# Performance work log

Hardware: AMD Instinct MI355X
Metric: run time of the kernel (lower is better)

The kernel has to match this reference:

```python
import jax, jax.numpy as jnp
from jax import lax
import numpy as np

DN = ('NCHW', 'OIHW', 'NCHW')
EPS = 1e-5


def conv(x, w, b, stride, pad):
    y = lax.conv_general_dilated(x, w, (stride, stride), [(pad, pad), (pad, pad)],
                                 dimension_numbers=DN)
    return y + b[None, :, None, None]


def conv_transpose(x, w, b):
    # torch ConvTranspose2d(k=4, s=2, p=1) == conv with lhs_dilation=2, pad=k-1-p=2
    y = lax.conv_general_dilated(x, w, (1, 1), [(2, 2), (2, 2)],
                                 lhs_dilation=(2, 2), dimension_numbers=DN)
    return y + b[None, :, None, None]


def group_norm(x, gamma, beta, groups):
    b, c, h, w = x.shape
    xg = x.reshape(b, groups, -1)
    mean = xg.mean(axis=2, keepdims=True)
    var = xg.var(axis=2, keepdims=True)
    xg = (xg - mean) * lax.rsqrt(var + EPS)
    x = xg.reshape(b, c, h, w)
    return x * gamma[None, :, None, None] + beta[None, :, None, None]


def silu(x):
    return x * jax.nn.sigmoid(x)


def setup_inputs() -> dict:
    key = jax.random.key(0)
    ks = iter(jax.random.split(key, 40))
    s = 0.05
    d = {}
    d['x'] = jax.random.normal(next(ks), (16, 3, 256, 256), dtype=jnp.float32)
    # encoder: 3->128->256->512 (k=4,s=2,p=1) each with GroupNorm(32)+SiLU, then 512->32 1x1
    chans = [(3, 128), (128, 256), (256, 512)]
    for i, (ci, co) in enumerate(chans):
        d[f'enc{i}_w'] = jax.random.normal(next(ks), (co, ci, 4, 4), dtype=jnp.float32) * s
        d[f'enc{i}_b'] = jnp.zeros((co,), jnp.float32)
        d[f'enc{i}_g'] = jnp.ones((co,), jnp.float32)
        d[f'enc{i}_bt'] = jnp.zeros((co,), jnp.float32)
    d['enc3_w'] = jax.random.normal(next(ks), (32, 512, 1, 1), dtype=jnp.float32) * s
    d['enc3_b'] = jnp.zeros((32,), jnp.float32)
    d['codebook'] = jax.random.normal(next(ks), (1024, 32), dtype=jnp.float32)
    # decoder: 32->512 1x1, then ConvT 512->256, 256->128 (GN+SiLU), ConvT 128->3 + tanh
    d['dec0_w'] = jax.random.normal(next(ks), (512, 32, 1, 1), dtype=jnp.float32) * s
    d['dec0_b'] = jnp.zeros((512,), jnp.float32)
    tchans = [(512, 256), (256, 128)]
    for i, (ci, co) in enumerate(tchans, start=1):
        d[f'dec{i}_w'] = jax.random.normal(next(ks), (co, ci, 4, 4), dtype=jnp.float32) * s
        d[f'dec{i}_b'] = jnp.zeros((co,), jnp.float32)
        d[f'dec{i}_g'] = jnp.ones((co,), jnp.float32)
        d[f'dec{i}_bt'] = jnp.zeros((co,), jnp.float32)
    d['dec3_w'] = jax.random.normal(next(ks), (3, 128, 4, 4), dtype=jnp.float32) * s
    d['dec3_b'] = jnp.zeros((3,), jnp.float32)
    return d


def reference(x, enc0_w, enc0_b, enc0_g, enc0_bt,
              enc1_w, enc1_b, enc1_g, enc1_bt,
              enc2_w, enc2_b, enc2_g, enc2_bt,
              enc3_w, enc3_b, codebook,
              dec0_w, dec0_b,
              dec1_w, dec1_b, dec1_g, dec1_bt,
              dec2_w, dec2_b, dec2_g, dec2_bt,
              dec3_w, dec3_b):
    # encoder
    h = silu(group_norm(conv(x, enc0_w, enc0_b, 2, 1), enc0_g, enc0_bt, 32))
    h = silu(group_norm(conv(h, enc1_w, enc1_b, 2, 1), enc1_g, enc1_bt, 32))
    h = silu(group_norm(conv(h, enc2_w, enc2_b, 2, 1), enc2_g, enc2_bt, 32))
    z = conv(h, enc3_w, enc3_b, 1, 0)          # [B, 32, 32, 32]
    b, c, hh, ww = z.shape
    zf = z.reshape(-1, c)                       # row-major flatten, as in original
    # squared-distance matrix [B*H*W, n_embeddings]
    d = (jnp.sum(zf * zf, axis=1, keepdims=True)
         + jnp.sum(codebook * codebook, axis=1)
         - 2.0 * zf @ codebook.T)
    idx = jnp.argmin(d, axis=1)
    q = codebook[idx].reshape(b, c, hh, ww)
    # decoder
    h = conv(q, dec0_w, dec0_b, 1, 0)
    h = silu(group_norm(conv_transpose(h, dec1_w, dec1_b), dec1_g, dec1_bt, 32))
    h = silu(group_norm(conv_transpose(h, dec2_w, dec2_b), dec2_g, dec2_bt, 32))
    recon = jnp.tanh(conv_transpose(h, dec3_w, dec3_b))
    return recon, q, idx
```

## Files before the change

### kernel.cpp

```cpp
#include <hip/hip_runtime.h>
#include <hip/hip_bf16.h>
#include <math.h>


#define EPS 1e-5f
typedef unsigned short ushort_t;
typedef unsigned int uint32;
typedef __attribute__((ext_vector_type(8))) short bf16x8;
typedef __attribute__((ext_vector_type(4))) float f32x4;
typedef __attribute__((ext_vector_type(4))) unsigned int u32x4;

__device__ __forceinline__ ushort_t f2bf(float x) {
    __hip_bfloat16 h = __float2bfloat16(x);
    return __builtin_bit_cast(ushort_t, h);
}
__device__ __forceinline__ float bf2f(ushort_t u) {
    __hip_bfloat16 h = __builtin_bit_cast(__hip_bfloat16, u);
    return __bfloat162float(h);
}
template <int NS>
__device__ __forceinline__ void splitNS(float x, ushort_t* p) {
    float r = x;
    #pragma unroll
    for (int s = 0; s < NS; ++s) {
        ushort_t u = f2bf(r);
        p[s] = u;
        if (s + 1 < NS) r -= bf2f(u);
    }
}

template <int Cout, int Cin>
__global__ __launch_bounds__(256) void wsplit_enc(
    const float* __restrict__ w, ushort_t* __restrict__ o)
{
    constexpr int KCH = Cin / 32, CB = Cout / 16;
    int idx = blockIdx.x * 256 + threadIdx.x;
    if (idx >= Cout * Cin * 16) return;
    int tap = idx & 15;
    int ci  = (idx >> 4) % Cin;
    int co  = (idx >> 4) / Cin;
    ushort_t sp[3];
    splitNS<3>(w[idx], sp);
    const int kc = ci >> 5, q = (ci >> 3) & 3, e = ci & 7;
    const int cb = co >> 4, l15 = co & 15;
    const int lane = q * 16 + l15;
    #pragma unroll
    for (int s = 0; s < 3; ++s)
        o[((((size_t)(s * 16 + tap) * KCH + kc) * CB + cb) * 64 + lane) * 8 + e] = sp[s];
}

template <int KCH, int CB>
__device__ __forceinline__ void ldaf2(bf16x8 (&dst)[2][3],
    const ushort_t* __restrict__ wsp_t, int kc, int tap)
{
    #pragma unroll
    for (int cf = 0; cf < 2; ++cf)
        #pragma unroll
        for (int s = 0; s < 3; ++s)
            dst[cf][s] = *(const bf16x8*)(wsp_t +
                ((size_t)((s * 16 + tap) * KCH + kc) * CB + cf) * 512);
}

template <int Cin, int Cout, int Hin, int Win>
__global__ __launch_bounds__(512, 4) void mfenc(
    const float* __restrict__ x, const ushort_t* __restrict__ wsp,
    const float* __restrict__ bias, float* __restrict__ y)
{
    constexpr int Hout = Hin / 2, Wout = Win / 2;
    constexpr int MB = 32;
    constexpr int MT = Wout / MB;
    constexpr int NCOL = 66;
    constexpr int KC = 32;
    constexpr int KCH = Cin / 32;
    constexpr int CB = Cout / 16;
    constexpr int BUFW = 3 * 4 * 4 * 68 * 8;
    __shared__ ushort_t Xs[BUFW];

    const int n  = blockIdx.z;
    const int oh = blockIdx.x / MT;
    const int mt = blockIdx.x % MT;
    const int M0 = mt * MB;
    const int co_base = blockIdx.y * 256;
    const int tid = threadIdx.x;
    const int wv = tid >> 6, lane = tid & 63;
    const int q = lane >> 4, l15 = lane & 15;
    const int co_w0 = co_base + wv * 32;
    const int cb0 = (co_base >> 4) + wv * 2;
    const ushort_t* __restrict__ wsp_t = wsp + ((size_t)cb0 * 64 + lane) * 8;

    int ro[4]; bool rv[4];
    #pragma unroll
    for (int k = 0; k < 4; ++k) {
        int r = 2 * oh - 1 + k;
        rv[k] = (r >= 0) && (r < Hin);
        ro[k] = rv[k] ? r : 0;
    }

    f32x4 acc[2][2];
    #pragma unroll
    for (int a = 0; a < 2; ++a)
        #pragma unroll
        for (int b = 0; b < 2; ++b) acc[a][b] = (f32x4){0.f, 0.f, 0.f, 0.f};

    const int p16  = tid >> 5;
    const int cg5  = tid & 31;
    const int sciq = p16 >> 2;
    const int cieP = p16 & 3;

    float a0[4][3], a1[4][3];

    auto stage_load = [&](int ci0) {
        const float* b0 = x + (size_t)(n * Cin + ci0 + 2 * p16) * Hin * Win;
        const float* b1 = b0 + (size_t)Hin * Win;
        #pragma unroll
        for (int r = 0; r < 4; ++r) {
            const float* rp0 = b0 + (size_t)ro[r] * Win;
            const float* rp1 = b1 + (size_t)ro[r] * Win;
            #pragma unroll
            for (int t = 0; t < 3; ++t) {
                const int c = cg5 + 32 * t;
                const int gc = 2 * M0 - 1 + c;
                const bool ok = rv[r] && (c < NCOL) && (gc >= 0) && (gc < Win);
                a0[r][t] = ok ? rp0[gc] : 0.f;
                a1[r][t] = ok ? rp1[gc] : 0.f;
            }
        }
    };
    auto stage_write = [&]() {
        uint32* __restrict__ dst32 = (uint32*)Xs;
        #pragma unroll
        for (int r = 0; r < 4; ++r)
            #pragma unroll
            for (int t = 0; t < 3; ++t) {
                const int c = cg5 + 32 * t;
                if (c < NCOL) {
                    ushort_t s0[3], s1[3];
                    splitNS<3>(a0[r][t], s0);
                    splitNS<3>(a1[r][t], s1);
                    const int cpos = (c >> 1) + (c & 1) * 34;
                    #pragma unroll
                    for (int s = 0; s < 3; ++s)
                        dst32[((((s * 4 + r) * 4 + sciq) * 68) + cpos) * 4 + cieP] =
                            (uint32)s0[s] | ((uint32)s1[s] << 16);
                }
            }
    };

    bf16x8 afA[2][3], afB[2][3];
    ldaf2<KCH, CB>(afA, wsp_t, 0, 0);

    stage_load(0);
    stage_write();
    __syncthreads();

    for (int kc = 0; kc < KCH; ++kc) {
        if (kc + 1 < KCH) stage_load((kc + 1) * KC);
        __builtin_amdgcn_sched_barrier(0);

        __builtin_amdgcn_s_setprio(1);
        #pragma unroll
        for (int tap = 0; tap < 16; ++tap) {
            bf16x8 (&cw)[2][3] = (tap & 1) ? afB : afA;
            bf16x8 (&nw)[2][3] = (tap & 1) ? afA : afB;
            if (tap < 15) {
                ldaf2<KCH, CB>(nw, wsp_t, kc, tap + 1);
            } else if (kc + 1 < KCH) {
                ldaf2<KCH, CB>(nw, wsp_t, kc + 1, 0);
            }

            const int kh = tap >> 2, kw = tap & 3;
            bf16x8 bx[2][3];
            const int cpbase = (kw >> 1) + (kw & 1) * 34;
            #pragma unroll
            for (int mf = 0; mf < 2; ++mf) {
                const int cpos = (mf * 16 + l15) + cpbase;
                #pragma unroll
                for (int s = 0; s < 3; ++s)
                    bx[mf][s] = *(const bf16x8*)(&Xs[((((s * 4 + kh) * 4 + q) * 68) + cpos) * 8]);
            }
            #pragma unroll
            for (int sa = 0; sa < 3; ++sa)
                #pragma unroll
                for (int sb = 0; sb < 3; ++sb) {
                    if (sa + sb >= 3) continue;
                    #pragma unroll
                    for (int cf = 0; cf < 2; ++cf)
                        #pragma unroll
                        for (int mf = 0; mf < 2; ++mf)
                            acc[cf][mf] = __builtin_amdgcn_mfma_f32_16x16x32_bf16(
                                cw[cf][sa], bx[mf][sb], acc[cf][mf], 0, 0, 0);
                }
        }
        __builtin_amdgcn_s_setprio(0);

        if (kc + 1 < KCH) {
            __syncthreads();
            stage_write();
            __syncthreads();
        }
    }

    #pragma unroll
    for (int cf = 0; cf < 2; ++cf)
        #pragma unroll
        for (int mf = 0; mf < 2; ++mf) {
            const int ow = M0 + mf * 16 + l15;
            #pragma unroll
            for (int rg = 0; rg < 4; ++rg) {
                const int co = co_w0 + cf * 16 + q * 4 + rg;
                y[(((size_t)n * Cout + co) * Hout + oh) * Wout + ow] =
                    acc[cf][mf][rg] + bias[co];
            }
        }
}

template <int Cout, int Cin>
__global__ __launch_bounds__(256) void wsplit_convt(
    const float* __restrict__ w, ushort_t* __restrict__ o)
{
    constexpr int KST = Cin / 8;
    constexpr int CB = Cout / 16;
    int idx = blockIdx.x * 256 + threadIdx.x;
    if (idx >= 4 * KST * CB * 512) return;
    const int e = idx & 7;
    const int lane = (idx >> 3) & 63;
    int rest = idx >> 9;
    const int cb = rest % CB; rest /= CB;
    const int kst = rest % KST;
    const int p = rest / KST;
    const int q = lane >> 4, l15 = lane & 15;
    const int co = cb * 16 + l15;
    const int kf = kst * 32 + q * 8 + e;
    const int ci = kf >> 2, a = (kf >> 1) & 1, b = kf & 1;
    const int di = p >> 1, dj = p & 1;
    const float v = w[(((size_t)co * Cin + ci) * 4 + (2 * a + di)) * 4 + (2 * b + dj)];
    o[idx] = f2bf(v);
}

template <int Cin, int Cout, int Hin, int Win, int CO_WAVES, int M_WAVES, int KC>
__global__ __launch_bounds__(256) void mfconvt(
    const float* __restrict__ x, const ushort_t* __restrict__ wsp,
    const float* __restrict__ bias, float* __restrict__ y)
{
    constexpr int NDp = Win / 2 + 2;
    constexpr int CO_B = CO_WAVES * 32;
    constexpr int KST = Cin / 8;
    constexpr int CB = Cout / 16;
    constexpr int KCH = Cin / KC;
    constexpr int SEGW = Win / 4;
    constexpr int SEGS = KC * 2 * SEGW;
    constexpr int NSEG = SEGS / 256;
    constexpr int BUFD = KC * 2 * 2 * NDp;
    static_assert(CO_WAVES * M_WAVES == 4, "4 waves");
    static_assert(M_WAVES * 32 == Win, "block spans full row");
    static_assert(KC % 8 == 0 && SEGS % 256 == 0, "seg mapping");
    static_assert((KC / 8) % 2 == 0, "even steps per chunk for wdbuf parity");
    __shared__ unsigned int Xs[2 * BUFD];

    const int bi = blockIdx.x;
    const int i  = bi >> 1;
    const int di = bi & 1;
    const int n = blockIdx.z;
    const int co_base = blockIdx.y * CO_B;
    const int tid = threadIdx.x;
    const int wv = tid >> 6, lane = tid & 63;
    const int cw = wv / M_WAVES, mw = wv % M_WAVES;
    const int co_w0 = co_base + cw * 32;
    const int cbw = (co_base >> 4) + cw * 2;
    const int m_w0 = mw * 32;
    const int q = lane >> 4, l15 = lane & 15;
    const ushort_t* __restrict__ wspL = wsp + (size_t)lane * 8;

    const int r0 = i - 1 + di, r1 = i + di;
    const bool v0 = (r0 >= 0), v1 = (r1 < Hin);
    const int r0c = v0 ? r0 : 0, r1c = v1 ? r1 : 0;

    f32x4 acc[2][2][2];
    #pragma unroll
    for (int a = 0; a < 2; ++a)
        #pragma unroll
        for (int b = 0; b < 2; ++b)
            #pragma unroll
            for (int d = 0; d < 2; ++d) acc[a][b][d] = (f32x4){0.f, 0.f, 0.f, 0.f};

    int sc0[NSEG], sci[NSEG], sA[NSEG], sgr[NSEG]; bool sok[NSEG];
    #pragma unroll
    for (int j = 0; j < NSEG; ++j) {
        const int seg = tid + 256 * j;
        sc0[j] = (seg % SEGW) * 4;
        const int rem = seg / SEGW;
        sA[j] = rem & 1;
        sci[j] = rem >> 1;
        sok[j] = sA[j] ? v1 : v0;
        sgr[j] = sA[j] ? r1c : r0c;
    }

    float sv[NSEG][5];

    auto stage_load = [&](int ci0) {
        #pragma unroll
        for (int j = 0; j < NSEG; ++j) {
            const float* rp = x + ((size_t)(n * Cin + ci0 + sci[j]) * Hin + sgr[j]) * Win;
            const int c0 = sc0[j];
            sv[j][0] = (sok[j] && c0 > 0) ? rp[c0 - 1] : 0.f;
            #pragma unroll
            for (int t = 1; t < 5; ++t) sv[j][t] = sok[j] ? rp[c0 + t - 1] : 0.f;
        }
    };
    auto stage_write = [&](int buf) {
        unsigned int* __restrict__ dst = (unsigned int*)Xs + buf * BUFD;
        #pragma unroll
        for (int j = 0; j < NSEG; ++j) {
            ushort_t sp[5];
            #pragma unroll
            for (int t = 0; t < 5; ++t) sp[t] = f2bf(sv[j][t]);
            const int c0 = sc0[j];
            const int base = (sci[j] * 2 + sA[j]) * 2 * NDp;
            dst[base + (c0 >> 1)]           = (unsigned)sp[1] | ((unsigned)sp[2] << 16);
            dst[base + (c0 >> 1) + 1]       = (unsigned)sp[3] | ((unsigned)sp[4] << 16);
            dst[base + NDp + (c0 >> 1)]     = (unsigned)sp[0] | ((unsigned)sp[1] << 16);
            dst[base + NDp + (c0 >> 1) + 1] = (unsigned)sp[2] | ((unsigned)sp[3] << 16);
            if (c0 == Win - 4)
                dst[base + NDp + (Win >> 1)] = (unsigned)sp[4];
        }
    };

    auto ldw = [&](bf16x8 (&dst)[2][2], int g) {
        #pragma unroll
        for (int dj = 0; dj < 2; ++dj)
            #pragma unroll
            for (int cf = 0; cf < 2; ++cf)
                dst[dj][cf] = *(const bf16x8*)(wspL +
                    (((size_t)(2 * di + dj) * KST + g) * CB + cbw + cf) * 512);
    };

    bf16x8 afA[2][2], afB[2][2];
    ldw(afA, 0);

    stage_load(0);
    stage_write(0);
    __syncthreads();

    for (int kcI = 0; kcI < KCH; ++kcI) {
        const int cur = kcI & 1;
        const unsigned int* __restrict__ Xr = (unsigned int*)Xs + cur * BUFD;

        if (kcI + 1 < KCH) stage_load((kcI + 1) * KC);
        __builtin_amdgcn_sched_barrier(0);

        __builtin_amdgcn_s_setprio(1);
        #pragma unroll
        for (int csi = 0; csi < KC / 8; ++csi) {
            bf16x8 (&cw_)[2][2] = (csi & 1) ? afB : afA;
            bf16x8 (&nw_)[2][2] = (csi & 1) ? afA : afB;
            const int g = kcI * (KC / 8) + csi;
            if (g + 1 < KST) ldw(nw_, g + 1);

            const int ciA = csi * 8 + q * 2;
            bf16x8 bfr[2][2];
            #pragma unroll
            for (int dj = 0; dj < 2; ++dj)
                #pragma unroll
                for (int mf = 0; mf < 2; ++mf) {
                    const int m = m_w0 + mf * 16 + l15;
                    const int c = m - 1 + dj;
                    const int copy = c & 1;
                    const int idx = (c + 1) >> 1;
                    u32x4 bd;
                    bd.x = Xr[((ciA)     * 2 + 0) * 2 * NDp + copy * NDp + idx];
                    bd.y = Xr[((ciA)     * 2 + 1) * 2 * NDp + copy * NDp + idx];
                    bd.z = Xr[((ciA + 1) * 2 + 0) * 2 * NDp + copy * NDp + idx];
                    bd.w = Xr[((ciA + 1) * 2 + 1) * 2 * NDp + copy * NDp + idx];
                    bfr[dj][mf] = __builtin_bit_cast(bf16x8, bd);
                }
            #pragma unroll
            for (int cf = 0; cf < 2; ++cf)
                #pragma unroll
                for (int mf = 0; mf < 2; ++mf)
                    #pragma unroll
                    for (int dj = 0; dj < 2; ++dj)
                        acc[cf][mf][dj] = __builtin_amdgcn_mfma_f32_16x16x32_bf16(
                            cw_[dj][cf], bfr[dj][mf], acc[cf][mf][dj], 0, 0, 0);
        }
        __builtin_amdgcn_s_setprio(0);

        if (kcI + 1 < KCH) {
            stage_write(cur ^ 1);
            __syncthreads();
        }
    }

    constexpr int Ho2 = Hin * 2, Wo2 = Win * 2;
    const int orow = 2 * i + di;
    #pragma unroll
    for (int cf = 0; cf < 2; ++cf)
        #pragma unroll
        for (int mf = 0; mf < 2; ++mf) {
            const int ocol0 = 2 * (m_w0 + mf * 16 + l15);
            #pragma unroll
            for (int rg = 0; rg < 4; ++rg) {
                const int co = co_w0 + cf * 16 + q * 4 + rg;
                const float b = bias[co];
                float2 o2;
                o2.x = acc[cf][mf][0][rg] + b;
                o2.y = acc[cf][mf][1][rg] + b;
                *(float2*)&y[(((size_t)n * Cout + co) * Ho2 + orow) * Wo2 + ocol0] = o2;
            }
        }
}

template <int Cin, int Cout, int Hin, int Win, int CO_T>
__global__ __launch_bounds__(256) void conv4s2_k(
    const float* __restrict__ x, const float* __restrict__ w,
    const float* __restrict__ bias, float* __restrict__ y)
{
    constexpr int Hout = Hin / 2, Wout = Win / 2, Wt = Wout / 4;
    const int n   = blockIdx.z;
    const int co0 = blockIdx.y * CO_T;
    const int local = blockIdx.x * 256 + threadIdx.x;
    const int wt = local & (Wt - 1);
    const int oh = local / Wt;
    const int iw0 = (wt << 3) - 1;
    const int ih0 = (oh << 1) - 1;

    const float* __restrict__ xn = x + (size_t)n * Cin * Hin * Win;
    const float* __restrict__ wb = w + (size_t)co0 * Cin * 16;

    const bool cL = (wt > 0);
    const bool cR = (wt < Wt - 1);

    float acc[CO_T][4];
    #pragma unroll
    for (int u = 0; u < CO_T; ++u)
        acc[u][0] = acc[u][1] = acc[u][2] = acc[u][3] = 0.f;

    bool rv[4]; int ro[4];
    #pragma unroll
    for (int k = 0; k < 4; ++k) {
        int r = ih0 + k;
        rv[k] = (r >= 0) && (r < Hin);
        ro[k] = rv[k] ? r : 0;
    }

    for (int ci = 0; ci < Cin; ++ci) {
        const float* xp = xn + (size_t)ci * Hin * Win;
        float xv[4][10];
        #pragma unroll
        for (int k = 0; k < 4; ++k) {
            const float* rp = xp + (size_t)ro[k] * Win;
            float4 m0 = *(const float4*)(rp + (wt << 3));
            float4 m1 = *(const float4*)(rp + (wt << 3) + 4);
            float e0 = cL ? rp[iw0] : 0.f;
            float e9 = cR ? rp[iw0 + 9] : 0.f;
            bool rk = rv[k];
            xv[k][0] = rk ? e0 : 0.f;
            xv[k][1] = rk ? m0.x : 0.f;
            xv[k][2] = rk ? m0.y : 0.f;
            xv[k][3] = rk ? m0.z : 0.f;
            xv[k][4] = rk ? m0.w : 0.f;
            xv[k][5] = rk ? m1.x : 0.f;
            xv[k][6] = rk ? m1.y : 0.f;
            xv[k][7] = rk ? m1.z : 0.f;
            xv[k][8] = rk ? m1.w : 0.f;
            xv[k][9] = rk ? e9 : 0.f;
        }
        #pragma unroll
        for (int u = 0; u < CO_T; ++u) {
            const float* wp = wb + ((size_t)u * Cin + ci) * 16;
            #pragma unroll
            for (int kh = 0; kh < 4; ++kh) {
                #pragma unroll
                for (int kw = 0; kw < 4; ++kw) {
                    float wv = wp[kh * 4 + kw];
                    acc[u][0] = fmaf(xv[kh][kw + 0], wv, acc[u][0]);
                    acc[u][1] = fmaf(xv[kh][kw + 2], wv, acc[u][1]);
                    acc[u][2] = fmaf(xv[kh][kw + 4], wv, acc[u][2]);
                    acc[u][3] = fmaf(xv[kh][kw + 6], wv, acc[u][3]);
                }
            }
        }
    }

    #pragma unroll
    for (int u = 0; u < CO_T; ++u) {
        float b = bias[co0 + u];
        float4 o;
        o.x = acc[u][0] + b; o.y = acc[u][1] + b;
        o.z = acc[u][2] + b; o.w = acc[u][3] + b;
        float* yp = y + (((size_t)(n * Cout + co0 + u)) * Hout + oh) * Wout + (wt << 2);
        *(float4*)yp = o;
    }
}

__global__ __launch_bounds__(256) void gn_stats(
    const float* __restrict__ y, float2* __restrict__ part,
    int HWshift, int grpC, int K)
{
    const int kblk = blockIdx.x;
    const int bg = blockIdx.y;
    const int b = bg >> 5, g = bg & 31;
    const int C = grpC << 5;
    const size_t base = ((size_t)b * C + (size_t)g * grpC) << HWshift;
    const int count4 = (grpC << HWshift) >> 2;
    const int chunk4 = count4 / K;
    const int ofs4 = kblk * chunk4;
    const float4* y4 = (const float4*)(y + base);

    float s = 0.f, ss = 0.f;
    for (int i = ofs4 + threadIdx.x; i < ofs4 + chunk4; i += 256) {
        float4 v = y4[i];
        s += v.x + v.y + v.z + v.w;
        ss = fmaf(v.x, v.x, ss); ss = fmaf(v.y, v.y, ss);
        ss = fmaf(v.z, v.z, ss); ss = fmaf(v.w, v.w, ss);
    }
    __shared__ float sh0[256];
    __shared__ float sh1[256];
    sh0[threadIdx.x] = s; sh1[threadIdx.x] = ss;
    __syncthreads();
    for (int off = 128; off > 0; off >>= 1) {
        if (threadIdx.x < off) {
            sh0[threadIdx.x] += sh0[threadIdx.x + off];
            sh1[threadIdx.x] += sh1[threadIdx.x + off];
        }
        __syncthreads();
    }
    if (threadIdx.x == 0) {
        float2 pp; pp.x = sh0[0]; pp.y = sh1[0];
        part[bg * K + kblk] = pp;
    }
}

__global__ __launch_bounds__(256) void gn_apply(
    float* __restrict__ y, const float* __restrict__ gamma,
    const float* __restrict__ beta, const float2* __restrict__ part,
    int HWshift, int grpC, int K)
{
    const int kblk = blockIdx.x;
    const int bg = blockIdx.y;
    const int b = bg >> 5, g = bg & 31;
    const int C = grpC << 5;
    const size_t base = ((size_t)b * C + (size_t)g * grpC) << HWshift;
    const int count4 = (grpC << HWshift) >> 2;
    const int chunk4 = count4 / K;
    const int ofs4 = kblk * chunk4;
    float4* y4 = (float4*)(y + base);

    float s = 0.f, ss = 0.f;
    for (int k = 0; k < K; ++k) {
        float2 pp = part[bg * K + k];
        s += pp.x; ss += pp.y;
    }
    const float inv = 1.f / (float)(count4 * 4);
    const float mean = s * inv;
    const float var = ss * inv - mean * mean;
    const float rstd = rsqrtf(var + EPS);

    const int HW4shift = HWshift - 2;
    for (int i = ofs4 + threadIdx.x; i < ofs4 + chunk4; i += 256) {
        int c = g * grpC + (i >> HW4shift);
        float ga = gamma[c], be = beta[c];
        float4 v = y4[i];
        float t0 = (v.x - mean) * rstd * ga + be;
        float t1 = (v.y - mean) * rstd * ga + be;
        float t2 = (v.z - mean) * rstd * ga + be;
        float t3 = (v.w - mean) * rstd * ga + be;
        v.x = t0 / (1.f + __expf(-t0));
        v.y = t1 / (1.f + __expf(-t1));
        v.z = t2 / (1.f + __expf(-t2));
        v.w = t3 / (1.f + __expf(-t3));
        y4[i] = v;
    }
}

template <int Cin, int Cout, int HW, int CO_T>
__global__ __launch_bounds__(256) void conv1x1_k(
    const float* __restrict__ x, const float* __restrict__ w,
    const float* __restrict__ bias, float* __restrict__ y)
{
    const int n = blockIdx.z;
    const int co0 = blockIdx.y * CO_T;
    const int s = blockIdx.x * 256 + threadIdx.x;
    const float* xp = x + (size_t)n * Cin * HW + s;

    float acc[CO_T];
    #pragma unroll
    for (int u = 0; u < CO_T; ++u) acc[u] = bias[co0 + u];

    for (int ci = 0; ci < Cin; ++ci) {
        float v = xp[(size_t)ci * HW];
        #pragma unroll
        for (int u = 0; u < CO_T; ++u)
            acc[u] = fmaf(v, w[(size_t)(co0 + u) * Cin + ci], acc[u]);
    }
    #pragma unroll
    for (int u = 0; u < CO_T; ++u)
        y[(size_t)(n * Cout + co0 + u) * HW + s] = acc[u];
}

__global__ __launch_bounds__(256) void cb_norm(
    const float* __restrict__ cb, float* __restrict__ cn)
{
    int j = blockIdx.x * 256 + threadIdx.x;
    const float* c = cb + (size_t)j * 32;
    float s = 0.f;
    #pragma unroll
    for (int k = 0; k < 32; ++k) s = fmaf(c[k], c[k], s);
    cn[j] = s;
}

__global__ __launch_bounds__(256) void vq_kernel(
    const float* __restrict__ z, const float* __restrict__ cb,
    const float* __restrict__ cn, float* __restrict__ q,
    float* __restrict__ idxf)
{
    const int row = blockIdx.x * 4 + (threadIdx.x >> 6);
    const int lane = threadIdx.x & 63;
    const float* zr = z + (size_t)row * 32;
    float zreg[32];
    #pragma unroll
    for (int k = 0; k < 32; ++k) zreg[k] = zr[k];
    float zn = 0.f;
    #pragma unroll
    for (int k = 0; k < 32; ++k) zn = fmaf(zreg[k], zreg[k], zn);

    float best = 3.4e38f;
    int bj = 0;
    for (int ii = 0; ii < 16; ++ii) {
        int j = lane * 16 + ii;
        const float* c = cb + (size_t)j * 32;
        float dot = 0.f;
        #pragma unroll
        for (int k = 0; k < 32; ++k) dot = fmaf(zreg[k], c[k], dot);
        float d = zn + cn[j] - 2.f * dot;
        if (d < best) { best = d; bj = j; }
    }
    #pragma unroll
    for (int off = 1; off < 64; off <<= 1) {
        float ob = __shfl_xor(best, off);
        int oj = __shfl_xor(bj, off);
        if (ob < best || (ob == best && oj < bj)) { best = ob; bj = oj; }
    }
    if (lane < 32) q[(size_t)row * 32 + lane] = cb[(size_t)bj * 32 + lane];
    if (lane == 0) idxf[row] = (float)bj;
}

template <int Cin, int CO_T, int CICHUNK>
__device__ __forceinline__ void stage_weights(
    const float* __restrict__ wb, int ci0, float4* __restrict__ lds4)
{
    constexpr int W4 = CICHUNK * CO_T * 4;
    for (int g4 = threadIdx.x; g4 < W4; g4 += blockDim.x) {
        int u = g4 / (CICHUNK * 4);
        int r4 = g4 - u * (CICHUNK * 4);
        lds4[g4] = ((const float4*)(wb + (size_t)u * Cin * 16 + (size_t)ci0 * 16))[r4];
    }
}

template <int Cin, int Cout, int Hin, int Win, int CO_T, int CICHUNK, bool TANH>
__global__ __launch_bounds__(256) void convt2_lds(
    const float* __restrict__ x, const float* __restrict__ w,
    const float* __restrict__ bias, float* __restrict__ y)
{
    constexpr int Wt2 = Win / 2;
    __shared__ float4 wlds[CICHUNK * CO_T * 4];

    const int n = blockIdx.z;
    const int co0 = blockIdx.y * CO_T;
    const int local = blockIdx.x * 256 + threadIdx.x;
    const int jt = local & (Wt2 - 1);
    const int i = local / Wt2;
    const int j0 = jt << 1;

    const float* __restrict__ xn = x + (size_t)n * Cin * Hin * Win;
    const float* __restrict__ wb = w + (size_t)co0 * Cin * 16;

    const bool rm0 = (i > 0), rm2 = (i + 1 < Hin);
    const bool cmL = (jt > 0), cmR = (jt < Wt2 - 1);
    const int ro0 = rm0 ? (i - 1) : 0;
    const int ro2 = rm2 ? (i + 1) : 0;

    float acc[CO_T][2][4];
    #pragma unroll
    for (int u = 0; u < CO_T; ++u)
        #pragma unroll
        for (int p = 0; p < 2; ++p)
            acc[u][p][0] = acc[u][p][1] = acc[u][p][2] = acc[u][p][3] = 0.f;

    for (int ci0 = 0; ci0 < Cin; ci0 += CICHUNK) {
        if (ci0) __syncthreads();
        stage_weights<Cin, CO_T, CICHUNK>(wb, ci0, wlds);
        __syncthreads();

        for (int cic = 0; cic < CICHUNK; ++cic) {
            const int ci = ci0 + cic;
            const float* xp = xn + (size_t)ci * Hin * Win;
            float xr[3][4];
            {
                const int rows[3] = {ro0, i, ro2};
                const bool rvn[3] = {rm0, true, rm2};
                #pragma unroll
                for (int r = 0; r < 3; ++r) {
                    const float* rp = xp + (size_t)rows[r] * Win;
                    float2 m = *(const float2*)(rp + j0);
                    float eL = cmL ? rp[j0 - 1] : 0.f;
                    float eR = cmR ? rp[j0 + 2] : 0.f;
                    bool rk = rvn[r];
                    xr[r][0] = rk ? eL : 0.f;
                    xr[r][1] = rk ? m.x : 0.f;
                    xr[r][2] = rk ? m.y : 0.f;
                    xr[r][3] = rk ? eR : 0.f;
                }
            }
            #pragma unroll
            for (int u = 0; u < CO_T; ++u) {
                const int wbase = (cic * CO_T + u) * 4;
                float4 wq0 = wlds[wbase + 0];
                float4 wq1 = wlds[wbase + 1];
                float4 wq2 = wlds[wbase + 2];
                float4 wq3 = wlds[wbase + 3];
                #pragma unroll
                for (int p = 0; p < 2; ++p) {
                    float x00 = xr[0][p], x01 = xr[0][p + 1], x02 = xr[0][p + 2];
                    float x10 = xr[1][p], x11 = xr[1][p + 1], x12 = xr[1][p + 2];
                    float x20 = xr[2][p], x21 = xr[2][p + 1], x22 = xr[2][p + 2];
                    float* a = acc[u][p];
                    a[0] = fmaf(x00, wq0.x, a[0]); a[0] = fmaf(x01, wq0.z, a[0]);
                    a[0] = fmaf(x10, wq2.x, a[0]); a[0] = fmaf(x11, wq2.z, a[0]);
                    a[1] = fmaf(x01, wq0.y, a[1]); a[1] = fmaf(x02, wq0.w, a[1]);
                    a[1] = fmaf(x11, wq2.y, a[1]); a[1] = fmaf(x12, wq2.w, a[1]);
                    a[2] = fmaf(x10, wq1.x, a[2]); a[2] = fmaf(x11, wq1.z, a[2]);
                    a[2] = fmaf(x20, wq3.x, a[2]); a[2] = fmaf(x21, wq3.z, a[2]);
                    a[3] = fmaf(x11, wq1.y, a[3]); a[3] = fmaf(x12, wq1.w, a[3]);
                    a[3] = fmaf(x21, wq3.y, a[3]); a[3] = fmaf(x22, wq3.w, a[3]);
                }
            }
        }
    }

    constexpr int Hout = Hin * 2, Wout = Win * 2;
    #pragma unroll
    for (int u = 0; u < CO_T; ++u) {
        float b = bias[co0 + u];
        float r00 = acc[u][0][0] + b, r01 = acc[u][0][1] + b;
        float r02 = acc[u][1][0] + b, r03 = acc[u][1][1] + b;
        float r10 = acc[u][0][2] + b, r11 = acc[u][0][3] + b;
        float r12 = acc[u][1][2] + b, r13 = acc[u][1][3] + b;
        if (TANH) {
            r00 = tanhf(r00); r01 = tanhf(r01); r02 = tanhf(r02); r03 = tanhf(r03);
            r10 = tanhf(r10); r11 = tanhf(r11); r12 = tanhf(r12); r13 = tanhf(r13);
        }
        float* yp = y + (((size_t)(n * Cout + co0 + u)) * Hout + (i << 1)) * Wout + (jt << 2);
        float4 o;
        o.x = r00; o.y = r01; o.z = r02; o.w = r03; *(float4*)yp = o;
        o.x = r10; o.y = r11; o.z = r12; o.w = r13; *(float4*)(yp + Wout) = o;
    }
}

extern "C" void kernel_launch(void* const* d_in, const int* in_sizes, int n_in,
                              void* d_out, int out_size, void* d_ws, size_t ws_size,
                              hipStream_t stream)
{
    const float* x       = (const float*)d_in[0];
    const float* enc0_w  = (const float*)d_in[1];
    const float* enc0_b  = (const float*)d_in[2];
    const float* enc0_g  = (const float*)d_in[3];
    const float* enc0_bt = (const float*)d_in[4];
    const float* enc1_w  = (const float*)d_in[5];
    const float* enc1_b  = (const float*)d_in[6];
    const float* enc1_g  = (const float*)d_in[7];
    const float* enc1_bt = (const float*)d_in[8];
    const float* enc2_w  = (const float*)d_in[9];
    const float* enc2_b  = (const float*)d_in[10];
    const float* enc2_g  = (const float*)d_in[11];
    const float* enc2_bt = (const float*)d_in[12];
    const float* enc3_w  = (const float*)d_in[13];
    const float* enc3_b  = (const float*)d_in[14];
    const float* codebook= (const float*)d_in[15];
    const float* dec0_w  = (const float*)d_in[16];
    const float* dec0_b  = (const float*)d_in[17];
    const float* dec1_w  = (const float*)d_in[18];
    const float* dec1_b  = (const float*)d_in[19];
    const float* dec1_g  = (const float*)d_in[20];
    const float* dec1_bt = (const float*)d_in[21];
    const float* dec2_w  = (const float*)d_in[22];
    const float* dec2_b  = (const float*)d_in[23];
    const float* dec2_g  = (const float*)d_in[24];
    const float* dec2_bt = (const float*)d_in[25];
    const float* dec3_w  = (const float*)d_in[26];
    const float* dec3_b  = (const float*)d_in[27];

    float* ws = (float*)d_ws;
    float*  A  = ws;
    float*  B  = ws + 33554432;
    float*  C  = ws + 50331648;
    float*  Z  = ws + 58720256;
    float*  CN = ws + 59244544;
    float2* GP = (float2*)(ws + 59245568);

    ushort_t* WE1 = (ushort_t*)C;
    ushort_t* WE2 = (ushort_t*)A;
    ushort_t* WD1 = (ushort_t*)C;
    ushort_t* WD2 = (ushort_t*)(C + 4194304);

    float* out   = (float*)d_out;
    float* recon = out;
    float* qbuf  = out + 3145728;
    float* idxf  = out + 3670016;

    const dim3 blk(256);
    const dim3 blk512(512);
    const int K = 16;
    const dim3 gngrid(K, 512);

    wsplit_enc<256, 128><<<dim3(2048), blk, 0, stream>>>(enc1_w, WE1);

    conv4s2_k<3, 128, 256, 256, 8><<<dim3(16, 16, 16), blk, 0, stream>>>(
        x, enc0_w, enc0_b, A);
    gn_stats<<<gngrid, blk, 0, stream>>>(A, GP, 14, 4, K);
    gn_apply<<<gngrid, blk, 0, stream>>>(A, enc0_g, enc0_bt, GP, 14, 4, K);

    mfenc<128, 256, 128, 128><<<dim3(128, 1, 16), blk512, 0, stream>>>(
        A, WE1, enc1_b, B);

    wsplit_enc<512, 256><<<dim3(8192), blk, 0, stream>>>(enc2_w, WE2);

    gn_stats<<<gngrid, blk, 0, stream>>>(B, GP, 12, 8, K);
    gn_apply<<<gngrid, blk, 0, stream>>>(B, enc1_g, enc1_bt, GP, 12, 8, K);

    mfenc<256, 512, 64, 64><<<dim3(32, 2, 16), blk512, 0, stream>>>(
        B, WE2, enc2_b, C);
    gn_stats<<<gngrid, blk, 0, stream>>>(C, GP, 10, 16, K);
    gn_apply<<<gngrid, blk, 0, stream>>>(C, enc2_g, enc2_bt, GP, 10, 16, K);

    conv1x1_k<512, 32, 1024, 8><<<dim3(4, 4, 16), blk, 0, stream>>>(
        C, enc3_w, enc3_b, Z);

    cb_norm<<<dim3(4), blk, 0, stream>>>(codebook, CN);
    vq_kernel<<<dim3(16384 / 4), blk, 0, stream>>>(Z, codebook, CN, qbuf, idxf);

    wsplit_convt<256, 512><<<dim3(8192), blk, 0, stream>>>(dec1_w, WD1);
    wsplit_convt<128, 256><<<dim3(2048), blk, 0, stream>>>(dec2_w, WD2);

    conv1x1_k<32, 512, 1024, 8><<<dim3(4, 64, 16), blk, 0, stream>>>(
        qbuf, dec0_w, dec0_b, A);

    mfconvt<512, 256, 32, 32, 4, 1, 32><<<dim3(64, 2, 16), blk, 0, stream>>>(
        A, WD1, dec1_b, B);
    gn_stats<<<gngrid, blk, 0, stream>>>(B, GP, 12, 8, K);
    gn_apply<<<gngrid, blk, 0, stream>>>(B, dec1_g, dec1_bt, GP, 12, 8, K);

    mfconvt<256, 128, 64, 64, 2, 2, 32><<<dim3(128, 2, 16), blk, 0, stream>>>(
        B, WD2, dec2_b, A);
    gn_stats<<<gngrid, blk, 0, stream>>>(A, GP, 14, 4, K);
    gn_apply<<<gngrid, blk, 0, stream>>>(A, dec2_g, dec2_bt, GP, 14, 4, K);

    convt2_lds<128, 3, 128, 128, 3, 128, true><<<dim3(32, 1, 16), blk, 0, stream>>>(
        A, dec3_w, dec3_b, recon);
}
```

Measured before the change: 2.102 ms.

## Compute two output rows per block in mfenc to reuse weight fragments

Each mfenc block now produces two adjacent output rows instead of one. It stages 6 input rows into LDS instead of 4 and doubles the accumulators, so every weight fragment loaded from global memory feeds twice as many MFMAs. The grids are halved to match. In exchange the kernel uses more registers and LDS (the occupancy hint of 4 is dropped) and launches fewer blocks, which may reduce occupancy and latency hiding.

```diff
diff --git a/kernel.cpp b/kernel.cpp
--- a/kernel.cpp
+++ b/kernel.cpp
@@ -62,7 +62,7 @@
 }
 
 template <int Cin, int Cout, int Hin, int Win>
-__global__ __launch_bounds__(512, 4) void mfenc(
+__global__ __launch_bounds__(512) void mfenc(
     const float* __restrict__ x, const ushort_t* __restrict__ wsp,
     const float* __restrict__ bias, float* __restrict__ y)
 {
@@ -73,11 +73,12 @@
     constexpr int KC = 32;
     constexpr int KCH = Cin / 32;
     constexpr int CB = Cout / 16;
-    constexpr int BUFW = 3 * 4 * 4 * 68 * 8;
+    constexpr int NR = 6;
+    constexpr int BUFW = 3 * NR * 4 * 68 * 8;
     __shared__ ushort_t Xs[BUFW];
 
     const int n  = blockIdx.z;
-    const int oh = blockIdx.x / MT;
+    const int oh0 = 2 * (blockIdx.x / MT);
     const int mt = blockIdx.x % MT;
     const int M0 = mt * MB;
     const int co_base = blockIdx.y * 256;
@@ -88,32 +89,34 @@
     const int cb0 = (co_base >> 4) + wv * 2;
     const ushort_t* __restrict__ wsp_t = wsp + ((size_t)cb0 * 64 + lane) * 8;
 
-    int ro[4]; bool rv[4];
-    #pragma unroll
-    for (int k = 0; k < 4; ++k) {
-        int r = 2 * oh - 1 + k;
+    int ro[NR]; bool rv[NR];
+    #pragma unroll
+    for (int k = 0; k < NR; ++k) {
+        int r = 2 * oh0 - 1 + k;
         rv[k] = (r >= 0) && (r < Hin);
         ro[k] = rv[k] ? r : 0;
     }
 
-    f32x4 acc[2][2];
+    f32x4 acc[2][2][2];
     #pragma unroll
     for (int a = 0; a < 2; ++a)
         #pragma unroll
-        for (int b = 0; b < 2; ++b) acc[a][b] = (f32x4){0.f, 0.f, 0.f, 0.f};
+        for (int b = 0; b < 2; ++b)
+            #pragma unroll
+            for (int h2 = 0; h2 < 2; ++h2) acc[a][b][h2] = (f32x4){0.f, 0.f, 0.f, 0.f};
 
     const int p16  = tid >> 5;
     const int cg5  = tid & 31;
     const int sciq = p16 >> 2;
     const int cieP = p16 & 3;
 
-    float a0[4][3], a1[4][3];
+    float a0[NR][3], a1[NR][3];
 
     auto stage_load = [&](int ci0) {
         const float* b0 = x + (size_t)(n * Cin + ci0 + 2 * p16) * Hin * Win;
         const float* b1 = b0 + (size_t)Hin * Win;
         #pragma unroll
-        for (int r = 0; r < 4; ++r) {
+        for (int r = 0; r < NR; ++r) {
             const float* rp0 = b0 + (size_t)ro[r] * Win;
             const float* rp1 = b1 + (size_t)ro[r] * Win;
             #pragma unroll
@@ -129,7 +132,7 @@
     auto stage_write = [&]() {
         uint32* __restrict__ dst32 = (uint32*)Xs;
         #pragma unroll
-        for (int r = 0; r < 4; ++r)
+        for (int r = 0; r < NR; ++r)
             #pragma unroll
             for (int t = 0; t < 3; ++t) {
                 const int c = cg5 + 32 * t;
@@ -140,7 +143,7 @@
                     const int cpos = (c >> 1) + (c & 1) * 34;
                     #pragma unroll
                     for (int s = 0; s < 3; ++s)
-                        dst32[((((s * 4 + r) * 4 + sciq) * 68) + cpos) * 4 + cieP] =
+                        dst32[((((s * NR + r) * 4 + sciq) * 68) + cpos) * 4 + cieP] =
                             (uint32)s0[s] | ((uint32)s1[s] << 16);
                 }
             }
@@ -169,14 +172,18 @@
             }
 
             const int kh = tap >> 2, kw = tap & 3;
-            bf16x8 bx[2][3];
+            bf16x8 bx[2][2][3];
             const int cpbase = (kw >> 1) + (kw & 1) * 34;
             #pragma unroll
-            for (int mf = 0; mf < 2; ++mf) {
-                const int cpos = (mf * 16 + l15) + cpbase;
+            for (int h2 = 0; h2 < 2; ++h2) {
+                const int row = kh + 2 * h2;
                 #pragma unroll
-                for (int s = 0; s < 3; ++s)
-                    bx[mf][s] = *(const bf16x8*)(&Xs[((((s * 4 + kh) * 4 + q) * 68) + cpos) * 8]);
+                for (int mf = 0; mf < 2; ++mf) {
+                    const int cpos = (mf * 16 + l15) + cpbase;
+                    #pragma unroll
+                    for (int s = 0; s < 3; ++s)
+                        bx[h2][mf][s] = *(const bf16x8*)(&Xs[((((s * NR + row) * 4 + q) * 68) + cpos) * 8]);
+                }
             }
             #pragma unroll
             for (int sa = 0; sa < 3; ++sa)
@@ -187,8 +194,10 @@
                     for (int cf = 0; cf < 2; ++cf)
                         #pragma unroll
                         for (int mf = 0; mf < 2; ++mf)
-                            acc[cf][mf] = __builtin_amdgcn_mfma_f32_16x16x32_bf16(
-                                cw[cf][sa], bx[mf][sb], acc[cf][mf], 0, 0, 0);
+                            #pragma unroll
+                            for (int h2 = 0; h2 < 2; ++h2)
+                                acc[cf][mf][h2] = __builtin_amdgcn_mfma_f32_16x16x32_bf16(
+                                    cw[cf][sa], bx[h2][mf][sb], acc[cf][mf][h2], 0, 0, 0);
                 }
         }
         __builtin_amdgcn_s_setprio(0);
@@ -206,10 +215,14 @@
         for (int mf = 0; mf < 2; ++mf) {
             const int ow = M0 + mf * 16 + l15;
             #pragma unroll
-            for (int rg = 0; rg < 4; ++rg) {
-                const int co = co_w0 + cf * 16 + q * 4 + rg;
-                y[(((size_t)n * Cout + co) * Hout + oh) * Wout + ow] =
-                    acc[cf][mf][rg] + bias[co];
+            for (int h2 = 0; h2 < 2; ++h2) {
+                const int oh = oh0 + h2;
+                #pragma unroll
+                for (int rg = 0; rg < 4; ++rg) {
+                    const int co = co_w0 + cf * 16 + q * 4 + rg;
+                    y[(((size_t)n * Cout + co) * Hout + oh) * Wout + ow] =
+                        acc[cf][mf][h2][rg] + bias[co];
+                }
             }
         }
 }
@@ -819,7 +832,7 @@
     gn_stats<<<gngrid, blk, 0, stream>>>(A, GP, 14, 4, K);
     gn_apply<<<gngrid, blk, 0, stream>>>(A, enc0_g, enc0_bt, GP, 14, 4, K);
 
-    mfenc<128, 256, 128, 128><<<dim3(128, 1, 16), blk512, 0, stream>>>(
+    mfenc<128, 256, 128, 128><<<dim3(64, 1, 16), blk512, 0, stream>>>(
         A, WE1, enc1_b, B);
 
     wsplit_enc<512, 256><<<dim3(8192), blk, 0, stream>>>(enc2_w, WE2);
@@ -827,7 +840,7 @@
     gn_stats<<<gngrid, blk, 0, stream>>>(B, GP, 12, 8, K);
     gn_apply<<<gngrid, blk, 0, stream>>>(B, enc1_g, enc1_bt, GP, 12, 8, K);
 
-    mfenc<256, 512, 64, 64><<<dim3(32, 2, 16), blk512, 0, stream>>>(
+    mfenc<256, 512, 64, 64><<<dim3(16, 2, 16), blk512, 0, stream>>>(
         B, WE2, enc2_b, C);
     gn_stats<<<gngrid, blk, 0, stream>>>(C, GP, 10, 16, K);
     gn_apply<<<gngrid, blk, 0, stream>>>(C, enc2_g, enc2_bt, GP, 10, 16, K);
```

New measurement: 3.502 ms. 66.6% more time.

## Pre-split enc2 activations to bf16 and stage via global_load_lds DMA

Applied to the files above, without the earlier changes.

Adds a separate kernel that converts the enc2 input activations into three bf16 split planes in a channel-packed layout. A new enc2 conv kernel then fills shared memory with global_load_lds direct-to-LDS copies, sending padding lanes to a zero buffer, instead of having each thread convert and stage. The intent is to take the per-block split and convert work out of the staging path and cut register and VGPR traffic. In exchange it adds a full pass that writes three bf16 planes to workspace, and it drops the occupancy hint from launch_bounds.

```diff
diff --git a/kernel.cpp b/kernel.cpp
--- a/kernel.cpp
+++ b/kernel.cpp
@@ -59,6 +59,41 @@
         for (int s = 0; s < 3; ++s)
             dst[cf][s] = *(const bf16x8*)(wsp_t +
                 ((size_t)((s * 16 + tap) * KCH + kc) * CB + cf) * 512);
+}
+
+template <int C, int H, int W>
+__global__ __launch_bounds__(256) void asplit_k(
+    const float* __restrict__ x, ushort_t* __restrict__ o,
+    ushort_t* __restrict__ zb)
+{
+    constexpr int C8 = C / 8, HW = H * W;
+    const int idx = blockIdx.x * 256 + threadIdx.x;
+    if (idx == 0) {
+        uint32* z = (uint32*)zb;
+        z[0] = 0u; z[1] = 0u; z[2] = 0u; z[3] = 0u;
+    }
+    const int w = idx % W;
+    const int h = (idx / W) % H;
+    const int kcq = (idx / HW) % C8;
+    const int n = idx / (HW * C8);
+
+    ushort_t gr[3][8];
+    #pragma unroll
+    for (int e = 0; e < 8; ++e) {
+        const float v = x[(size_t)(n * C + kcq * 8 + e) * HW + h * W + w];
+        ushort_t sp[3];
+        splitNS<3>(v, sp);
+        gr[0][e] = sp[0]; gr[1][e] = sp[1]; gr[2][e] = sp[2];
+    }
+    #pragma unroll
+    for (int s = 0; s < 3; ++s) {
+        u32x4 ov;
+        ov.x = (uint32)gr[s][0] | ((uint32)gr[s][1] << 16);
+        ov.y = (uint32)gr[s][2] | ((uint32)gr[s][3] << 16);
+        ov.z = (uint32)gr[s][4] | ((uint32)gr[s][5] << 16);
+        ov.w = (uint32)gr[s][6] | ((uint32)gr[s][7] << 16);
+        *(u32x4*)&o[((((size_t)s * 16 + n) * C8 + kcq) * HW + (size_t)h * W + w) * 8] = ov;
+    }
 }
 
 template <int Cin, int Cout, int Hin, int Win>
@@ -196,6 +231,139 @@
         if (kc + 1 < KCH) {
             __syncthreads();
             stage_write();
+            __syncthreads();
+        }
+    }
+
+    #pragma unroll
+    for (int cf = 0; cf < 2; ++cf)
+        #pragma unroll
+        for (int mf = 0; mf < 2; ++mf) {
+            const int ow = M0 + mf * 16 + l15;
+            #pragma unroll
+            for (int rg = 0; rg < 4; ++rg) {
+                const int co = co_w0 + cf * 16 + q * 4 + rg;
+                y[(((size_t)n * Cout + co) * Hout + oh) * Wout + ow] =
+                    acc[cf][mf][rg] + bias[co];
+            }
+        }
+}
+
+template <int Cin, int Cout, int Hin, int Win>
+__global__ __launch_bounds__(512) void mfenc_dma(
+    const ushort_t* __restrict__ xs, const ushort_t* __restrict__ zb,
+    const ushort_t* __restrict__ wsp, const float* __restrict__ bias,
+    float* __restrict__ y)
+{
+    constexpr int Hout = Hin / 2, Wout = Win / 2;
+    constexpr int MB = 32;
+    constexpr int MT = Wout / MB;
+    constexpr int KC = 32;
+    constexpr int KCH = Cin / 32;
+    constexpr int CB = Cout / 16;
+    constexpr int C8 = Cin / 8;
+    constexpr int NG = 3 * 4 * 4 * 68;
+    constexpr int BUFW = NG * 8;
+    __shared__ ushort_t Xs[BUFW];
+
+    const int n  = blockIdx.z;
+    const int oh = blockIdx.x / MT;
+    const int mt = blockIdx.x % MT;
+    const int M0 = mt * MB;
+    const int co_base = blockIdx.y * 256;
+    const int tid = threadIdx.x;
+    const int wv = tid >> 6, lane = tid & 63;
+    const int q = lane >> 4, l15 = lane & 15;
+    const int co_w0 = co_base + wv * 32;
+    const int cb0 = (co_base >> 4) + wv * 2;
+    const ushort_t* __restrict__ wsp_t = wsp + ((size_t)cb0 * 64 + lane) * 8;
+
+    int ro[4]; bool rv[4];
+    #pragma unroll
+    for (int k = 0; k < 4; ++k) {
+        int r = 2 * oh - 1 + k;
+        rv[k] = (r >= 0) && (r < Hin);
+        ro[k] = rv[k] ? r : 0;
+    }
+
+    f32x4 acc[2][2];
+    #pragma unroll
+    for (int a = 0; a < 2; ++a)
+        #pragma unroll
+        for (int b = 0; b < 2; ++b) acc[a][b] = (f32x4){0.f, 0.f, 0.f, 0.f};
+
+    auto dma_stage = [&](int kc) {
+        #pragma unroll
+        for (int j = 0; j < (NG + 511) / 512; ++j) {
+            const int g = tid + 512 * j;
+            if (g < NG) {
+                const int cpos = g % 68;
+                int rest = g / 68;
+                const int ciq = rest & 3;
+                rest >>= 2;
+                const int r = rest & 3;
+                const int s = rest >> 2;
+                const int c = (cpos < 34) ? (cpos << 1) : (((cpos - 34) << 1) | 1);
+                const int gc = 2 * M0 - 1 + c;
+                const bool ok = rv[r] && (c < 66) && (gc >= 0) && (gc < Win);
+                const ushort_t* gp = ok
+                    ? xs + ((((size_t)s * 16 + n) * C8 + (kc * 4 + ciq)) * (Hin * Win)
+                            + (size_t)ro[r] * Win + gc) * 8
+                    : zb;
+                __builtin_amdgcn_global_load_lds(
+                    (const __attribute__((address_space(1))) uint32*)gp,
+                    (__attribute__((address_space(3))) uint32*)(&Xs[(size_t)g * 8]),
+                    16, 0, 0);
+            }
+        }
+    };
+
+    bf16x8 afA[2][3], afB[2][3];
+    ldaf2<KCH, CB>(afA, wsp_t, 0, 0);
+
+    dma_stage(0);
+    __syncthreads();
+
+    for (int kc = 0; kc < KCH; ++kc) {
+        __builtin_amdgcn_s_setprio(1);
+        #pragma unroll
+        for (int tap = 0; tap < 16; ++tap) {
+            bf16x8 (&cw)[2][3] = (tap & 1) ? afB : afA;
+            bf16x8 (&nw)[2][3] = (tap & 1) ? afA : afB;
+            if (tap < 15) {
+                ldaf2<KCH, CB>(nw, wsp_t, kc, tap + 1);
+            } else if (kc + 1 < KCH) {
+                ldaf2<KCH, CB>(nw, wsp_t, kc + 1, 0);
+            }
+
+            const int kh = tap >> 2, kw = tap & 3;
+            bf16x8 bx[2][3];
+            const int cpbase = (kw >> 1) + (kw & 1) * 34;
+            #pragma unroll
+            for (int mf = 0; mf < 2; ++mf) {
+                const int cpos = (mf * 16 + l15) + cpbase;
+                #pragma unroll
+                for (int s = 0; s < 3; ++s)
+                    bx[mf][s] = *(const bf16x8*)(&Xs[((((s * 4 + kh) * 4 + q) * 68) + cpos) * 8]);
+            }
+            #pragma unroll
+            for (int sa = 0; sa < 3; ++sa)
+                #pragma unroll
+                for (int sb = 0; sb < 3; ++sb) {
+                    if (sa + sb >= 3) continue;
+                    #pragma unroll
+                    for (int cf = 0; cf < 2; ++cf)
+                        #pragma unroll
+                        for (int mf = 0; mf < 2; ++mf)
+                            acc[cf][mf] = __builtin_amdgcn_mfma_f32_16x16x32_bf16(
+                                cw[cf][sa], bx[mf][sb], acc[cf][mf], 0, 0, 0);
+                }
+        }
+        __builtin_amdgcn_s_setprio(0);
+
+        if (kc + 1 < KCH) {
+            __syncthreads();
+            dma_stage(kc + 1);
             __syncthreads();
         }
     }
@@ -796,9 +964,11 @@
     float*  Z  = ws + 58720256;
     float*  CN = ws + 59244544;
     float2* GP = (float2*)(ws + 59245568);
+    ushort_t* ZB = (ushort_t*)(ws + 59261952);
 
     ushort_t* WE1 = (ushort_t*)C;
     ushort_t* WE2 = (ushort_t*)A;
+    ushort_t* BSP = WE2 + 6291456;
     ushort_t* WD1 = (ushort_t*)C;
     ushort_t* WD2 = (ushort_t*)(C + 4194304);
 
@@ -827,8 +997,10 @@
     gn_stats<<<gngrid, blk, 0, stream>>>(B, GP, 12, 8, K);
     gn_apply<<<gngrid, blk, 0, stream>>>(B, enc1_g, enc1_bt, GP, 12, 8, K);
 
-    mfenc<256, 512, 64, 64><<<dim3(32, 2, 16), blk512, 0, stream>>>(
-        B, WE2, enc2_b, C);
+    asplit_k<256, 64, 64><<<dim3(8192), blk, 0, stream>>>(B, BSP, ZB);
+
+    mfenc_dma<256, 512, 64, 64><<<dim3(32, 2, 16), blk512, 0, stream>>>(
+        BSP, ZB, WE2, enc2_b, C);
     gn_stats<<<gngrid, blk, 0, stream>>>(C, GP, 10, 16, K);
     gn_apply<<<gngrid, blk, 0, stream>>>(C, enc2_g, enc2_bt, GP, 10, 16, K);
 
```

Measured after the change: 2.186 ms. 1.04x slower.
